# Kernel optimization log

Measured on AMD Instinct MI355X. Metric: run time of the kernel, lower is better.

## Reference

```python
import jax, jax.numpy as jnp
import numpy as np

B, S, D, E, H, TOPK = 4, 1024, 512, 8, 1536, 2
NORM_EPS = 1e-5

def _ln(x, w, b, eps=1e-5):
    m = jnp.mean(x, -1, keepdims=True)
    v = jnp.var(x, -1, keepdims=True)  # biased var, as torch LayerNorm
    return (x - m) * jax.lax.rsqrt(v + eps) * w + b

def _modulate(x, shift, scale):
    return x * (1 + scale[:, None, :]) + shift[:, None, :]

def setup_inputs() -> dict:
    key = jax.random.key(0)
    ks = jax.random.split(key, 14)
    s = 0.02
    return dict(
        x=jax.random.normal(ks[0], (B, S, D), jnp.float32),
        c=jax.random.normal(ks[1], (B, D), jnp.float32),
        W_ada=jax.random.normal(ks[2], (D, 6 * D), jnp.float32) * s,
        b_ada=jax.random.normal(ks[3], (6 * D,), jnp.float32) * 0.1,
        Wq=jax.random.normal(ks[4], (D, D), jnp.float32) * s,
        Wk=jax.random.normal(ks[5], (D, D), jnp.float32) * s,
        Wv=jax.random.normal(ks[6], (D, D), jnp.float32) * s,
        Wo=jax.random.normal(ks[7], (D, D), jnp.float32) * s,
        qn_w=jnp.ones((D,), jnp.float32), qn_b=jnp.zeros((D,), jnp.float32),
        kn_w=jnp.ones((D,), jnp.float32), kn_b=jnp.zeros((D,), jnp.float32),
        an_w=jnp.ones((D,), jnp.float32), an_b=jnp.zeros((D,), jnp.float32),
        fn_w=jnp.ones((D,), jnp.float32), fn_b=jnp.zeros((D,), jnp.float32),
        Wr=jax.random.normal(ks[8], (D, E), jnp.float32) * s,
        br=jnp.zeros((E,), jnp.float32),
        W1=jax.random.normal(ks[9], (E, D, H), jnp.float32) * s,
        W2=jax.random.normal(ks[10], (E, H, D), jnp.float32) * s,
        W3=jax.random.normal(ks[11], (E, D, H), jnp.float32) * s,
    )

def reference(x, c, W_ada, b_ada, Wq, Wk, Wv, Wo, qn_w, qn_b, kn_w, kn_b,
              an_w, an_b, fn_w, fn_b, Wr, br, W1, W2, W3):
    # adaLN conditioning: SiLU -> Linear -> 6 chunks
    mods = jax.nn.silu(c) @ W_ada + b_ada          # (B, 6D)
    sh_msa, sc_msa, g_msa, sh_mlp, sc_mlp, g_mlp = jnp.split(mods, 6, axis=1)

    # Attention (source attends over the FEATURE dim: scores are (B, D, D))
    h = _modulate(_ln(x, an_w, an_b, NORM_EPS), sh_msa, sc_msa)
    q = _ln(h @ Wq, qn_w, qn_b)
    k = _ln(h @ Wk, kn_w, kn_b)
    v = h @ Wv
    scores = jnp.einsum('bsd,bse->bde', q, k)      # (B, D, D), no 1/sqrt scale (as source)
    A = jax.nn.softmax(scores, axis=-1)
    attn = jnp.einsum('bde,bse->bsd', A, v) @ Wo   # (B, S, D)
    x = x + g_msa[:, None, :] * attn

    # MoE feed-forward (top-2 routing; output REPLACES x, no residual/gate per source)
    xm = _modulate(_ln(x, fn_w, fn_b, NORM_EPS), sh_mlp, sc_mlp)
    logits = xm @ Wr + br                          # (B, S, E)
    # F.normalize default dim=1 -> L2 normalize over the SEQUENCE axis (faithful)
    nrm = jnp.sqrt(jnp.sum(logits * logits, axis=1, keepdims=True))
    logits = logits / jnp.maximum(nrm, 1e-12)
    probs = jax.nn.softmax(logits, axis=-1)        # (B, S, E)
    vals, idx = jax.lax.top_k(probs, TOPK)

    T = B * S
    xf = xm.reshape(T, D)
    # dense combine weights: zero for unselected experts (same math as gather/scatter-add)
    wden = jnp.zeros((T, E), xf.dtype).at[jnp.arange(T)[:, None], idx.reshape(T, TOPK)].set(vals.reshape(T, TOPK))
    h1 = jnp.einsum('td,edh->teh', xf, W1)
    h3 = jnp.einsum('td,edh->teh', xf, W3)
    y = jnp.einsum('teh,ehd->ted', jnp.sin(h1) * h3, W2)  # sin-gated FFN per expert
    moe = jnp.einsum('ted,te->td', y, wden).reshape(B, S, D)

    avg = probs.mean(axis=0)                       # mean over batch dim only (faithful): (S, E)
    aux = jnp.sum((1.0 / E - avg) ** 2)
    return moe, aux
```

## Files before the change

kernel.cpp:

```cpp
#include <hip/hip_runtime.h>
#include <math.h>

#define NB 4
#define NS 1024
#define ND 512
#define NE 8
#define NH 1536
#define NT 4096
#define D6 3072

typedef _Float16 half_t;
typedef _Float16 f16x8 __attribute__((ext_vector_type(8)));
typedef _Float16 f16x4 __attribute__((ext_vector_type(4)));
typedef float    f32x4 __attribute__((ext_vector_type(4)));

#define LDH 40
#define LDC 136
#define TM_MAX 71

__device__ __forceinline__ void gld16(const void* g, void* l) {
  __builtin_amdgcn_global_load_lds((const __attribute__((address_space(1))) char*)g,
                                   (__attribute__((address_space(3))) char*)l, 16, 0, 0);
}

__device__ __forceinline__ int resolve_tile(const int* __restrict__ offs, int t,
                                            int& e_out, int& m0_out) {
  int acc = 0, found = 0, ee = 0, mm = 0;
  #pragma unroll
  for (int q = 0; q < NE; ++q) {
    int ne_q = offs[q + 1] - offs[q];
    int te = (ne_q + 127) >> 7;
    if (!found && t < acc + te) { ee = q; mm = (t - acc) << 7; found = 1; }
    acc += te;
  }
  e_out = ee; m0_out = mm;
  return found;
}

__global__ __launch_bounds__(256) void k_ada(const float* __restrict__ c,
    const float* __restrict__ Wada, const float* __restrict__ bada,
    float* __restrict__ mods)
{
  __shared__ float sc[ND];
  __shared__ float part[256];
  int tid = threadIdx.x;
  int blk = blockIdx.x;
  int o0 = blk * 64;
  int b = o0 / D6;
  int j0 = o0 - b * D6;
  for (int d = tid; d < ND; d += 256) {
    float v = c[b * ND + d];
    sc[d] = v / (1.f + expf(-v));
  }
  __syncthreads();
  int j = j0 + (tid & 63);
  int kc = tid >> 6;
  float acc = 0.f;
  #pragma unroll 8
  for (int d = kc * 128; d < kc * 128 + 128; ++d)
    acc += sc[d] * Wada[(size_t)d * D6 + j];
  part[tid] = acc;
  __syncthreads();
  if (tid < 64) {
    float r = part[tid] + part[tid + 64] + part[tid + 128] + part[tid + 192]
            + bada[j0 + tid];
    mods[b * D6 + j0 + tid] = r;
  }
}

__global__ __launch_bounds__(256) void k_lnmod(const float* X, int xstride,
    float* Yf, half_t* Yh, half_t* Yl, int ystride,
    const float* __restrict__ w, const float* __restrict__ b,
    const float* __restrict__ mods, int sh_off, int sc_off,
    const float* __restrict__ Wr, const float* __restrict__ br,
    float* __restrict__ logits)
{
  __shared__ float red[16];
  __shared__ float red2[32];
  int tid = threadIdx.x;
  int row = blockIdx.x;
  int batch = row >> 10;
  const float* xr = X + (size_t)row * xstride;
  float x0 = xr[tid], x1 = xr[tid + 256];
  float s = x0 + x1, q = x0 * x0 + x1 * x1;
  #pragma unroll
  for (int off = 32; off > 0; off >>= 1) { s += __shfl_down(s, off, 64); q += __shfl_down(q, off, 64); }
  if ((tid & 63) == 0) { red[tid >> 6] = s; red[8 + (tid >> 6)] = q; }
  __syncthreads();
  if (tid == 0) {
    float S = red[0] + red[1] + red[2] + red[3];
    float Q = red[8] + red[9] + red[10] + red[11];
    float mean = S * (1.f / (float)ND);
    float var = Q * (1.f / (float)ND) - mean * mean;
    red[0] = mean; red[1] = rsqrtf(var + 1e-5f);
  }
  __syncthreads();
  float mean = red[0], rstd = red[1];
  int d0 = tid, d1 = tid + 256;
  float y0 = (x0 - mean) * rstd * w[d0] + b[d0];
  float y1 = (x1 - mean) * rstd * w[d1] + b[d1];
  if (mods) {
    const float* mb = mods + batch * D6;
    y0 = y0 * (1.f + mb[sc_off + d0]) + mb[sh_off + d0];
    y1 = y1 * (1.f + mb[sc_off + d1]) + mb[sh_off + d1];
  }
  size_t o0 = (size_t)row * ystride + d0, o1 = (size_t)row * ystride + d1;
  if (Yf) { Yf[o0] = y0; Yf[o1] = y1; }
  if (Yh) {
    half_t h0 = (half_t)y0, h1 = (half_t)y1;
    Yh[o0] = h0; Yh[o1] = h1;
    if (Yl) { Yl[o0] = (half_t)(y0 - (float)h0); Yl[o1] = (half_t)(y1 - (float)h1); }
  }
  if (Wr) {
    float p[8];
    float4 wa = *(const float4*)(Wr + d0 * 8);
    float4 wb = *(const float4*)(Wr + d0 * 8 + 4);
    float4 wc = *(const float4*)(Wr + d1 * 8);
    float4 wd = *(const float4*)(Wr + d1 * 8 + 4);
    p[0] = y0 * wa.x + y1 * wc.x; p[1] = y0 * wa.y + y1 * wc.y;
    p[2] = y0 * wa.z + y1 * wc.z; p[3] = y0 * wa.w + y1 * wc.w;
    p[4] = y0 * wb.x + y1 * wd.x; p[5] = y0 * wb.y + y1 * wd.y;
    p[6] = y0 * wb.z + y1 * wd.z; p[7] = y0 * wb.w + y1 * wd.w;
    #pragma unroll
    for (int off = 32; off > 0; off >>= 1)
      #pragma unroll
      for (int e = 0; e < 8; ++e) p[e] += __shfl_down(p[e], off, 64);
    if ((tid & 63) == 0) {
      #pragma unroll
      for (int e = 0; e < 8; ++e) red2[(tid >> 6) * 8 + e] = p[e];
    }
    __syncthreads();
    if (tid < 8)
      logits[(size_t)row * 8 + tid] = red2[tid] + red2[8 + tid] + red2[16 + tid]
                                    + red2[24 + tid] + br[tid];
  }
}

__global__ __launch_bounds__(256) void k_lnqk(float* QKV,
    const float* __restrict__ qw, const float* __restrict__ qb,
    const float* __restrict__ kw, const float* __restrict__ kb)
{
  __shared__ float red[16];
  int tid = threadIdx.x;
  int row = blockIdx.x >> 1;
  int h = blockIdx.x & 1;
  const float* w = h ? kw : qw;
  const float* b = h ? kb : qb;
  float* xr = QKV + (size_t)row * 1536 + h * 512;
  float x0 = xr[tid], x1 = xr[tid + 256];
  float s = x0 + x1, q = x0 * x0 + x1 * x1;
  #pragma unroll
  for (int off = 32; off > 0; off >>= 1) { s += __shfl_down(s, off, 64); q += __shfl_down(q, off, 64); }
  if ((tid & 63) == 0) { red[tid >> 6] = s; red[8 + (tid >> 6)] = q; }
  __syncthreads();
  if (tid == 0) {
    float S = red[0] + red[1] + red[2] + red[3];
    float Q = red[8] + red[9] + red[10] + red[11];
    float mean = S * (1.f / (float)ND);
    float var = Q * (1.f / (float)ND) - mean * mean;
    red[0] = mean; red[1] = rsqrtf(var + 1e-5f);
  }
  __syncthreads();
  float mean = red[0], rstd = red[1];
  xr[tid]       = (x0 - mean) * rstd * w[tid] + b[tid];
  xr[tid + 256] = (x1 - mean) * rstd * w[tid + 256] + b[tid + 256];
}

__global__ __launch_bounds__(256) void k_tsplit2(const float* __restrict__ QKV,
    half_t* __restrict__ H0, half_t* __restrict__ L0)
{
  __shared__ float tile[32][33];
  int z = blockIdx.z;
  half_t* outH = H0 + (size_t)z * 4194304;
  half_t* outL = L0 + (size_t)z * 4194304;
  int col0 = z * 512;
  int s0 = blockIdx.x * 32, c0 = blockIdx.y * 32;
  int tid = threadIdx.x;
  int r = tid >> 5, c = tid & 31;
  #pragma unroll
  for (int p = 0; p < 4; ++p)
    tile[r + p * 8][c] = QKV[(size_t)(s0 + r + p * 8) * 1536 + col0 + c0 + c];
  __syncthreads();
  #pragma unroll
  for (int p = 0; p < 4; ++p) {
    float v = tile[c][r + p * 8];
    half_t h = (half_t)v;
    size_t o = (size_t)(c0 + r + p * 8) * NT + s0 + c;
    outH[o] = h; outL[o] = (half_t)(v - (float)h);
  }
}

__global__ __launch_bounds__(256) void k_wsplit4(const float* __restrict__ Wq,
    const float* __restrict__ Wk, const float* __restrict__ Wv,
    const float* __restrict__ Wo, half_t* __restrict__ outH, half_t* __restrict__ outL)
{
  __shared__ float tile[32][33];
  int z = blockIdx.z;
  const float* W = (z == 0) ? Wq : (z == 1) ? Wk : (z == 2) ? Wv : Wo;
  int rowoff = z * 512;
  int k0 = blockIdx.x * 32, n0 = blockIdx.y * 32;
  int tid = threadIdx.x;
  int r = tid >> 5, c = tid & 31;
  #pragma unroll
  for (int p = 0; p < 4; ++p)
    tile[r + p * 8][c] = W[(size_t)(k0 + r + p * 8) * ND + n0 + c];
  __syncthreads();
  #pragma unroll
  for (int p = 0; p < 4; ++p) {
    float v = tile[c][r + p * 8];
    half_t h = (half_t)v;
    size_t o = (size_t)(rowoff + n0 + r + p * 8) * ND + k0 + c;
    outH[o] = h; outL[o] = (half_t)(v - (float)h);
  }
}

__global__ __launch_bounds__(256) void k_vsplit(const float* __restrict__ QKV,
    half_t* __restrict__ Vh, half_t* __restrict__ Vl)
{
  int i = blockIdx.x * 256 + threadIdx.x;
  int s = i >> 7, c = (i & 127) * 4;
  float4 v = *(const float4*)(QKV + (size_t)s * 1536 + 1024 + c);
  f16x4 h, l;
  h[0] = (half_t)v.x; l[0] = (half_t)(v.x - (float)h[0]);
  h[1] = (half_t)v.y; l[1] = (half_t)(v.y - (float)h[1]);
  h[2] = (half_t)v.z; l[2] = (half_t)(v.z - (float)h[2]);
  h[3] = (half_t)v.w; l[3] = (half_t)(v.w - (float)h[3]);
  *(f16x4*)(Vh + (size_t)s * ND + c) = h;
  *(f16x4*)(Vl + (size_t)s * ND + c) = l;
}

template<int MODE>
__global__ __launch_bounds__(256) void k_gemm_hl(
    const half_t* __restrict__ Ah, const half_t* __restrict__ Al, long long sAz,
    const half_t* __restrict__ Bh, const half_t* __restrict__ Bl, long long sBz,
    int lda, int ldb, int K,
    float* __restrict__ Cf, half_t* __restrict__ Ch, half_t* __restrict__ Cl,
    long long sCz, int ldc,
    const float* __restrict__ xres, const float* __restrict__ mods)
{
  int z = blockIdx.z;
  int m0 = blockIdx.x * 128, n0 = blockIdx.y * 128;
  __shared__ __align__(16) char smem[40960];
  half_t* Ash = (half_t*)smem;
  half_t* Asl = (half_t*)(smem + 10240);
  half_t* Bsh = (half_t*)(smem + 20480);
  half_t* Bsl = (half_t*)(smem + 30720);
  int tid = threadIdx.x;
  int lane = tid & 63, w = tid >> 6;
  int wm = (w >> 1) * 64, wn = (w & 1) * 64;
  int qd = lane >> 4, md = lane & 15;
  int rA0 = tid >> 2, sA0 = (tid & 3) * 8;
  int rA1 = rA0 + 64;

  const half_t* pAh0 = Ah + z * sAz + (size_t)(m0 + rA0) * lda + sA0;
  const half_t* pAh1 = Ah + z * sAz + (size_t)(m0 + rA1) * lda + sA0;
  const half_t* pAl0 = Al + z * sAz + (size_t)(m0 + rA0) * lda + sA0;
  const half_t* pAl1 = Al + z * sAz + (size_t)(m0 + rA1) * lda + sA0;
  const half_t* pBh0 = Bh + z * sBz + (size_t)(n0 + rA0) * ldb + sA0;
  const half_t* pBh1 = Bh + z * sBz + (size_t)(n0 + rA1) * ldb + sA0;
  const half_t* pBl0 = Bl + z * sBz + (size_t)(n0 + rA0) * ldb + sA0;
  const half_t* pBl1 = Bl + z * sBz + (size_t)(n0 + rA1) * ldb + sA0;

  f32x4 acc[4][4];
  #pragma unroll
  for (int i = 0; i < 4; ++i)
    #pragma unroll
    for (int j = 0; j < 4; ++j)
      #pragma unroll
      for (int p = 0; p < 4; ++p) acc[i][j][p] = 0.f;

  f16x8 rah0 = *(const f16x8*)pAh0, rah1 = *(const f16x8*)pAh1;
  f16x8 ral0 = *(const f16x8*)pAl0, ral1 = *(const f16x8*)pAl1;
  f16x8 rbh0 = *(const f16x8*)pBh0, rbh1 = *(const f16x8*)pBh1;
  f16x8 rbl0 = *(const f16x8*)pBl0, rbl1 = *(const f16x8*)pBl1;

  int iters = K >> 5;
  #pragma unroll 1
  for (int it = 0; it < iters; ++it) {
    __syncthreads();
    *(f16x8*)(Ash + rA0 * LDH + sA0) = rah0;
    *(f16x8*)(Ash + rA1 * LDH + sA0) = rah1;
    *(f16x8*)(Asl + rA0 * LDH + sA0) = ral0;
    *(f16x8*)(Asl + rA1 * LDH + sA0) = ral1;
    *(f16x8*)(Bsh + rA0 * LDH + sA0) = rbh0;
    *(f16x8*)(Bsh + rA1 * LDH + sA0) = rbh1;
    *(f16x8*)(Bsl + rA0 * LDH + sA0) = rbl0;
    *(f16x8*)(Bsl + rA1 * LDH + sA0) = rbl1;
    __syncthreads();
    if (it < iters - 1) {
      int k1 = (it + 1) * 32;
      rah0 = *(const f16x8*)(pAh0 + k1); rah1 = *(const f16x8*)(pAh1 + k1);
      ral0 = *(const f16x8*)(pAl0 + k1); ral1 = *(const f16x8*)(pAl1 + k1);
      rbh0 = *(const f16x8*)(pBh0 + k1); rbh1 = *(const f16x8*)(pBh1 + k1);
      rbl0 = *(const f16x8*)(pBl0 + k1); rbl1 = *(const f16x8*)(pBl1 + k1);
    }
    f16x8 ah[4], al[4], bh[4], bl[4];
    #pragma unroll
    for (int i = 0; i < 4; ++i) {
      ah[i] = *(const f16x8*)(Ash + (wm + 16 * i + md) * LDH + qd * 8);
      al[i] = *(const f16x8*)(Asl + (wm + 16 * i + md) * LDH + qd * 8);
    }
    #pragma unroll
    for (int j = 0; j < 4; ++j) {
      bh[j] = *(const f16x8*)(Bsh + (wn + 16 * j + md) * LDH + qd * 8);
      bl[j] = *(const f16x8*)(Bsl + (wn + 16 * j + md) * LDH + qd * 8);
    }
    #pragma unroll
    for (int i = 0; i < 4; ++i)
      #pragma unroll
      for (int j = 0; j < 4; ++j) {
        acc[i][j] = __builtin_amdgcn_mfma_f32_16x16x32_f16(ah[i], bh[j], acc[i][j], 0, 0, 0);
        acc[i][j] = __builtin_amdgcn_mfma_f32_16x16x32_f16(ah[i], bl[j], acc[i][j], 0, 0, 0);
        acc[i][j] = __builtin_amdgcn_mfma_f32_16x16x32_f16(al[i], bh[j], acc[i][j], 0, 0, 0);
      }
  }

  if (MODE == 1) {
    half_t* Cs = (half_t*)smem;
    __syncthreads();
    #pragma unroll
    for (int i = 0; i < 4; ++i)
      #pragma unroll
      for (int j = 0; j < 4; ++j)
        #pragma unroll
        for (int p = 0; p < 4; ++p)
          Cs[(wm + 16 * i + qd * 4 + p) * LDC + wn + 16 * j + md] = (half_t)acc[i][j][p];
    __syncthreads();
    #pragma unroll
    for (int it2 = 0; it2 < 8; ++it2) {
      int chunk = it2 * 256 + tid;
      int r = chunk >> 4, c8 = (chunk & 15) * 8;
      *(f16x8*)(Ch + z * sCz + (size_t)(m0 + r) * ldc + n0 + c8) = *(const f16x8*)(Cs + r * LDC + c8);
    }
    __syncthreads();
    #pragma unroll
    for (int i = 0; i < 4; ++i)
      #pragma unroll
      for (int j = 0; j < 4; ++j)
        #pragma unroll
        for (int p = 0; p < 4; ++p) {
          float v = acc[i][j][p];
          half_t h = (half_t)v;
          Cs[(wm + 16 * i + qd * 4 + p) * LDC + wn + 16 * j + md] = (half_t)(v - (float)h);
        }
    __syncthreads();
    #pragma unroll
    for (int it2 = 0; it2 < 8; ++it2) {
      int chunk = it2 * 256 + tid;
      int r = chunk >> 4, c8 = (chunk & 15) * 8;
      *(f16x8*)(Cl + z * sCz + (size_t)(m0 + r) * ldc + n0 + c8) = *(const f16x8*)(Cs + r * LDC + c8);
    }
  } else {
    #pragma unroll
    for (int i = 0; i < 4; ++i)
      #pragma unroll
      for (int p = 0; p < 4; ++p) {
        int r = m0 + wm + 16 * i + qd * 4 + p;
        float* cp = Cf + z * sCz + (size_t)r * ldc + n0 + wn + md;
        if (MODE == 2) {
          int batch = r >> 10;
          const float* mb = mods + batch * D6 + 2 * ND;
          const float* xp = xres + (size_t)r * ldc + n0 + wn + md;
          #pragma unroll
          for (int j = 0; j < 4; ++j) {
            int col = wn + md + 16 * j;
            cp[16 * j] = xp[16 * j] + mb[n0 + col] * acc[i][j][p];
          }
        } else {
          #pragma unroll
          for (int j = 0; j < 4; ++j) cp[16 * j] = acc[i][j][p];
        }
      }
  }
}

__global__ __launch_bounds__(256) void k_softmax512_sum4(const float* __restrict__ SC4,
    half_t* __restrict__ Ph, half_t* __restrict__ Pl)
{
  __shared__ float red[16];
  int tid = threadIdx.x;
  int row = blockIdx.x;
  int b = row >> 9, d = row & 511;
  const float* r0 = SC4 + ((size_t)(b * 4 + 0) << 18) + (size_t)d * ND;
  const float* r1 = SC4 + ((size_t)(b * 4 + 1) << 18) + (size_t)d * ND;
  const float* r2 = SC4 + ((size_t)(b * 4 + 2) << 18) + (size_t)d * ND;
  const float* r3 = SC4 + ((size_t)(b * 4 + 3) << 18) + (size_t)d * ND;
  float x0 = r0[tid] + r1[tid] + r2[tid] + r3[tid];
  float x1 = r0[tid + 256] + r1[tid + 256] + r2[tid + 256] + r3[tid + 256];
  float m = fmaxf(x0, x1);
  #pragma unroll
  for (int off = 32; off > 0; off >>= 1) m = fmaxf(m, __shfl_down(m, off, 64));
  if ((tid & 63) == 0) red[tid >> 6] = m;
  __syncthreads();
  if (tid == 0) red[0] = fmaxf(fmaxf(red[0], red[1]), fmaxf(red[2], red[3]));
  __syncthreads();
  m = red[0];
  float e0 = expf(x0 - m), e1 = expf(x1 - m);
  float s = e0 + e1;
  #pragma unroll
  for (int off = 32; off > 0; off >>= 1) s += __shfl_down(s, off, 64);
  if ((tid & 63) == 0) red[8 + (tid >> 6)] = s;
  __syncthreads();
  if (tid == 0) red[8] = red[8] + red[9] + red[10] + red[11];
  __syncthreads();
  float inv = 1.f / red[8];
  float p0 = e0 * inv, p1 = e1 * inv;
  size_t base = (size_t)row * ND;
  half_t h0 = (half_t)p0, h1 = (half_t)p1;
  Ph[base + tid] = h0;       Pl[base + tid] = (half_t)(p0 - (float)h0);
  Ph[base + tid + 256] = h1; Pl[base + tid + 256] = (half_t)(p1 - (float)h1);
}

__global__ __launch_bounds__(256) void k_colnorm(const float* __restrict__ logits,
    float* __restrict__ nrm, int* __restrict__ cnt)
{
  __shared__ float red[8];
  int tid = threadIdx.x;
  if (blockIdx.x == 0 && tid < 16) cnt[tid] = 0;
  int b = blockIdx.x >> 3, e = blockIdx.x & 7;
  float acc = 0.f;
  for (int s = tid; s < NS; s += 256) {
    float l = logits[((size_t)(b << 10) + s) * NE + e];
    acc += l * l;
  }
  #pragma unroll
  for (int off = 32; off > 0; off >>= 1) acc += __shfl_down(acc, off, 64);
  if ((tid & 63) == 0) red[tid >> 6] = acc;
  __syncthreads();
  if (tid == 0) nrm[b * NE + e] = sqrtf(red[0] + red[1] + red[2] + red[3]);
}

__global__ __launch_bounds__(256) void k_top2(const float* __restrict__ logits,
    const float* __restrict__ nrm, float* __restrict__ probs,
    float* __restrict__ wsel, int* __restrict__ isel, int* __restrict__ cnt)
{
  int t = blockIdx.x * 256 + threadIdx.x;
  int b = t >> 10;
  float p[NE];
  float mx = -1e30f;
  #pragma unroll
  for (int e = 0; e < NE; ++e) {
    float l = logits[t * NE + e] / fmaxf(nrm[b * NE + e], 1e-12f);
    p[e] = l;
    mx = fmaxf(mx, l);
  }
  float s = 0.f;
  #pragma unroll
  for (int e = 0; e < NE; ++e) { p[e] = expf(p[e] - mx); s += p[e]; }
  float inv = 1.f / s;
  #pragma unroll
  for (int e = 0; e < NE; ++e) { p[e] *= inv; probs[t * NE + e] = p[e]; }
  int i1 = 0;
  #pragma unroll
  for (int e = 1; e < NE; ++e) if (p[e] > p[i1]) i1 = e;
  int i2 = (i1 == 0) ? 1 : 0;
  #pragma unroll
  for (int e = 0; e < NE; ++e) if (e != i1 && p[e] > p[i2]) i2 = e;
  wsel[t * 2] = p[i1]; wsel[t * 2 + 1] = p[i2];
  isel[t * 2] = i1;    isel[t * 2 + 1] = i2;
  atomicAdd(&cnt[i1], 1); atomicAdd(&cnt[i2], 1);
}

__global__ void k_scan(const int* __restrict__ cnt, int* __restrict__ offs)
{
  if (threadIdx.x == 0) {
    int a = 0;
    for (int e = 0; e < NE; ++e) { offs[e] = a; a += cnt[e]; }
    offs[NE] = a;
  }
}

__global__ __launch_bounds__(256) void k_fill(const int* __restrict__ isel,
    const int* __restrict__ offs, int* __restrict__ cnt2,
    int* __restrict__ list, int* __restrict__ inv)
{
  int idx = blockIdx.x * 256 + threadIdx.x;
  int e = isel[idx];
  int pos = atomicAdd(&cnt2[e], 1);
  int slot = offs[e] + pos;
  list[slot] = idx >> 1;
  inv[idx] = slot;
}

__global__ __launch_bounds__(256) void k_aux(const float* __restrict__ probs,
    float* __restrict__ outAux)
{
  __shared__ float red[8];
  int tid = threadIdx.x;
  float acc = 0.f;
  for (int s = tid; s < NS; s += 256) {
    #pragma unroll
    for (int e = 0; e < NE; ++e) {
      float a = probs[(size_t)s * NE + e] + probs[(size_t)(NS + s) * NE + e]
              + probs[(size_t)(2 * NS + s) * NE + e] + probs[(size_t)(3 * NS + s) * NE + e];
      float d = 0.125f - a * 0.25f;
      acc += d * d;
    }
  }
  #pragma unroll
  for (int off = 32; off > 0; off >>= 1) acc += __shfl_down(acc, off, 64);
  if ((tid & 63) == 0) red[tid >> 6] = acc;
  __syncthreads();
  if (tid == 0) *outAux = red[0] + red[1] + red[2] + red[3];
}

__global__ __launch_bounds__(256) void k_tcast13(const float* __restrict__ W1,
    const float* __restrict__ W3, half_t* __restrict__ W1t, half_t* __restrict__ W3t)
{
  __shared__ float tile[32][33];
  int z = blockIdx.z;
  int sel = z >> 3, e = z & 7;
  const float* We = (sel ? W3 : W1) + (size_t)e * ND * NH;
  half_t* Wte = (sel ? W3t : W1t) + (size_t)e * ND * NH;
  int k0 = blockIdx.x * 32, n0 = blockIdx.y * 32;
  int tid = threadIdx.x;
  int r = tid >> 5, c = tid & 31;
  #pragma unroll
  for (int p = 0; p < 4; ++p)
    tile[r + p * 8][c] = We[(size_t)(k0 + r + p * 8) * NH + n0 + c];
  __syncthreads();
  #pragma unroll
  for (int p = 0; p < 4; ++p)
    Wte[(size_t)(n0 + r + p * 8) * ND + k0 + c] = (half_t)tile[c][r + p * 8];
}

__global__ __launch_bounds__(256) void k_tcastW2(const float* __restrict__ W,
    half_t* __restrict__ Wt)
{
  __shared__ float tile[32][33];
  const float* We = W + (size_t)blockIdx.z * NH * ND;
  half_t* Wte = Wt + (size_t)blockIdx.z * NH * ND;
  int k0 = blockIdx.x * 32, n0 = blockIdx.y * 32;
  int tid = threadIdx.x;
  int r = tid >> 5, c = tid & 31;
  #pragma unroll
  for (int p = 0; p < 4; ++p)
    tile[r + p * 8][c] = We[(size_t)(k0 + r + p * 8) * ND + n0 + c];
  __syncthreads();
  #pragma unroll
  for (int p = 0; p < 4; ++p)
    Wte[(size_t)(n0 + r + p * 8) * NH + k0 + c] = (half_t)tile[c][r + p * 8];
}

__global__ __launch_bounds__(256, 3) void k_ffn_fused(const half_t* __restrict__ xmh,
    const half_t* __restrict__ W1t, const half_t* __restrict__ W3t,
    const int* __restrict__ list, const int* __restrict__ offs,
    half_t* __restrict__ gate)
{
  int bx = blockIdx.x;
  int n0 = (bx % 12) * 128;
  int t  = bx / 12;
  int e, m0;
  if (!resolve_tile(offs, t, e, m0)) return;
  int base = offs[e], ne = offs[e + 1] - base;

  __shared__ __align__(16) char smem[49664];
  half_t* Sh = (half_t*)smem;
  int* rowt = (int*)(smem + 49152);
  int tid = threadIdx.x;
  if (tid < 128) {
    int rr = m0 + tid;
    rowt[tid] = (rr < ne) ? list[base + rr] : 0;
  }
  __syncthreads();

  int lane = tid & 63, w = tid >> 6;
  int wm = (w >> 1) * 64, wn = (w & 1) * 64;
  int qd = lane >> 4, md = lane & 15;
  int rA0 = tid >> 2;
  int sw = (((tid & 3) ^ ((tid >> 3) & 3)) << 3);
  int tok0 = rowt[rA0], tok1 = rowt[rA0 + 64];

  const half_t* gA0  = xmh + (size_t)tok0 * ND + sw;
  const half_t* gA1  = xmh + (size_t)tok1 * ND + sw;
  const half_t* gB10 = W1t + ((size_t)e * NH + n0 + rA0) * ND + sw;
  const half_t* gB11 = gB10 + (size_t)64 * ND;
  const half_t* gB30 = W3t + ((size_t)e * NH + n0 + rA0) * ND + sw;
  const half_t* gB31 = gB30 + (size_t)64 * ND;

  char* dA  = smem + w * 1024;
  char* dB1 = smem + 16384 + w * 1024;
  char* dB3 = smem + 32768 + w * 1024;

  f32x4 acc1[4][4], acc3[4][4];
  #pragma unroll
  for (int i = 0; i < 4; ++i)
    #pragma unroll
    for (int j = 0; j < 4; ++j)
      #pragma unroll
      for (int p = 0; p < 4; ++p) { acc1[i][j][p] = 0.f; acc3[i][j][p] = 0.f; }

  int swq  = ((qd ^ ((md >> 1) & 3)) << 3);
  int aoff = (wm + md) * 32 + swq;
  int boff = (wn + md) * 32 + swq;

#define FFN_STAGE(p, kk) do { int kb_ = (kk); int pb_ = (p) * 8192;          \
    gld16(gA0  + kb_, dA  + pb_); gld16(gA1  + kb_, dA  + pb_ + 4096);       \
    gld16(gB10 + kb_, dB1 + pb_); gld16(gB11 + kb_, dB1 + pb_ + 4096);       \
    gld16(gB30 + kb_, dB3 + pb_); gld16(gB31 + kb_, dB3 + pb_ + 4096); } while (0)

  FFN_STAGE(0, 0);
  asm volatile("s_waitcnt vmcnt(0)\ns_barrier" ::: "memory");
  int cur = 0;
  #pragma unroll 1
  for (int it = 0; it < 16; ++it) {
    if (it + 1 < 16) FFN_STAGE(cur ^ 1, (it + 1) * 32);
    const half_t* As  = Sh + cur * 4096;
    const half_t* B1s = Sh + 8192  + cur * 4096;
    const half_t* B3s = Sh + 16384 + cur * 4096;
    f16x8 a[4];
    #pragma unroll
    for (int i = 0; i < 4; ++i) a[i] = *(const f16x8*)(As + aoff + i * 512);
    #pragma unroll
    for (int j = 0; j < 4; ++j) {
      f16x8 b1 = *(const f16x8*)(B1s + boff + j * 512);
      f16x8 b3 = *(const f16x8*)(B3s + boff + j * 512);
      #pragma unroll
      for (int i = 0; i < 4; ++i) {
        acc1[i][j] = __builtin_amdgcn_mfma_f32_16x16x32_f16(a[i], b1, acc1[i][j], 0, 0, 0);
        acc3[i][j] = __builtin_amdgcn_mfma_f32_16x16x32_f16(a[i], b3, acc3[i][j], 0, 0, 0);
      }
    }
    asm volatile("s_waitcnt vmcnt(0)\ns_barrier" ::: "memory");
    cur ^= 1;
  }
#undef FFN_STAGE

  half_t* Cs = (half_t*)smem;
  #pragma unroll
  for (int i = 0; i < 4; ++i)
    #pragma unroll
    for (int j = 0; j < 4; ++j)
      #pragma unroll
      for (int p = 0; p < 4; ++p) {
        int rr = wm + 16 * i + qd * 4 + p;
        int cc = wn + 16 * j + md;
        Cs[rr * LDC + cc] = (half_t)(__sinf(acc1[i][j][p]) * acc3[i][j][p]);
      }
  __syncthreads();
  #pragma unroll
  for (int it = 0; it < 8; ++it) {
    int chunk = it * 256 + tid;
    int rr = chunk >> 4, c8 = (chunk & 15) * 8;
    if (m0 + rr < ne) {
      *(f16x8*)(gate + (size_t)(base + m0 + rr) * NH + n0 + c8) = *(const f16x8*)(Cs + rr * LDC + c8);
    }
  }
}

__global__ __launch_bounds__(256, 4) void k_moe2_mfma(const half_t* __restrict__ gate,
    const half_t* __restrict__ W2t, const int* __restrict__ offs,
    float* __restrict__ P)
{
  int bx = blockIdx.x;
  int n0 = (bx & 3) * 128;
  int t = bx >> 2;
  int e, m0;
  if (!resolve_tile(offs, t, e, m0)) return;
  int base = offs[e], ne = offs[e + 1] - base;

  __shared__ __align__(16) char smem[32768];
  half_t* Sh = (half_t*)smem;
  int tid = threadIdx.x;
  int lane = tid & 63, w = tid >> 6;
  int wm = (w >> 1) * 64, wn = (w & 1) * 64;
  int qd = lane >> 4, md = lane & 15;
  int rA0 = tid >> 2;
  int sw = (((tid & 3) ^ ((tid >> 3) & 3)) << 3);

  int ar0 = m0 + rA0;      if (ar0 >= ne) ar0 = ne - 1;
  int ar1 = m0 + rA0 + 64; if (ar1 >= ne) ar1 = ne - 1;
  const half_t* gA0 = gate + (size_t)(base + ar0) * NH + sw;
  const half_t* gA1 = gate + (size_t)(base + ar1) * NH + sw;
  const half_t* gB0 = W2t + ((size_t)e * ND + n0 + rA0) * NH + sw;
  const half_t* gB1 = gB0 + (size_t)64 * NH;

  char* dA = smem + w * 1024;
  char* dB = smem + 16384 + w * 1024;

  f32x4 acc[4][4];
  #pragma unroll
  for (int i = 0; i < 4; ++i)
    #pragma unroll
    for (int j = 0; j < 4; ++j)
      #pragma unroll
      for (int p = 0; p < 4; ++p) acc[i][j][p] = 0.f;

  int swq  = ((qd ^ ((md >> 1) & 3)) << 3);
  int aoff = (wm + md) * 32 + swq;
  int boff = (wn + md) * 32 + swq;

#define MOE2_STAGE(p, kk) do { int kb_ = (kk); int pb_ = (p) * 8192;         \
    gld16(gA0 + kb_, dA + pb_); gld16(gA1 + kb_, dA + pb_ + 4096);           \
    gld16(gB0 + kb_, dB + pb_); gld16(gB1 + kb_, dB + pb_ + 4096); } while (0)

  MOE2_STAGE(0, 0);
  asm volatile("s_waitcnt vmcnt(0)\ns_barrier" ::: "memory");
  int cur = 0;
  #pragma unroll 1
  for (int it = 0; it < 48; ++it) {
    if (it + 1 < 48) MOE2_STAGE(cur ^ 1, (it + 1) * 32);
    const half_t* As = Sh + cur * 4096;
    const half_t* Bs = Sh + 8192 + cur * 4096;
    f16x8 a[4];
    #pragma unroll
    for (int i = 0; i < 4; ++i) a[i] = *(const f16x8*)(As + aoff + i * 512);
    #pragma unroll
    for (int j = 0; j < 4; ++j) {
      f16x8 b = *(const f16x8*)(Bs + boff + j * 512);
      #pragma unroll
      for (int i = 0; i < 4; ++i)
        acc[i][j] = __builtin_amdgcn_mfma_f32_16x16x32_f16(a[i], b, acc[i][j], 0, 0, 0);
    }
    asm volatile("s_waitcnt vmcnt(0)\ns_barrier" ::: "memory");
    cur ^= 1;
  }
#undef MOE2_STAGE

  #pragma unroll
  for (int i = 0; i < 4; ++i)
    #pragma unroll
    for (int p = 0; p < 4; ++p) {
      int gr = m0 + wm + 16 * i + qd * 4 + p;
      if (gr < ne) {
        float* pp = P + (size_t)(base + gr) * ND + n0 + wn + md;
        #pragma unroll
        for (int j = 0; j < 4; ++j)
          pp[16 * j] = acc[i][j][p];
      }
    }
}

__global__ __launch_bounds__(256) void k_moe_reduce(const float* __restrict__ P,
    const int* __restrict__ inv, const float* __restrict__ wsel,
    float* __restrict__ out)
{
  int i = blockIdx.x * 256 + threadIdx.x;
  int t = i >> 7, d4 = i & 127;
  int s1 = inv[t * 2], s2 = inv[t * 2 + 1];
  float w1 = wsel[t * 2], w2 = wsel[t * 2 + 1];
  const float4* P4 = (const float4*)P;
  float4 a = P4[(size_t)s1 * 128 + d4];
  float4 b = P4[(size_t)s2 * 128 + d4];
  float4 o;
  o.x = w1 * a.x + w2 * b.x;
  o.y = w1 * a.y + w2 * b.y;
  o.z = w1 * a.z + w2 * b.z;
  o.w = w1 * a.w + w2 * b.w;
  ((float4*)out)[i] = o;
}

static const size_t BO_MODS  = 0;
static const size_t BO_HH    = 65536;
static const size_t BO_HL2   = 4259840;
static const size_t BO_PH    = 4259840;
static const size_t BO_PL    = 6357056;
static const size_t BO_WALLH = 8454144;
static const size_t BO_WALLL = 10551296;
static const size_t BO_QKV   = 12648448;
static const size_t BO_A0H   = 12648448;
static const size_t BO_A0L   = 16842752;
static const size_t BO_SC4   = 21037056;
static const size_t BO_X2    = 21037056;
static const size_t BO_XM    = 29425664;
static const size_t BO_QTH   = 37814272;
static const size_t BO_QTL   = 42008576;
static const size_t BO_KTH   = 46202880;
static const size_t BO_KTL   = 50397184;
static const size_t BO_VH    = 54591488;
static const size_t BO_VL    = 58785792;
static const size_t BO_W1T   = 37814272;
static const size_t BO_XMH   = 50397184;
static const size_t BO_W3T   = 65536;
static const size_t BO_GATE  = 12648448;
static const size_t BO_W2T   = 65536;
static const size_t BO_P     = 37814272;
static const size_t BO_LOGI  = 62980096;
static const size_t BO_NRM   = 63111168;
static const size_t BO_PROB  = 63111296;
static const size_t BO_WSEL  = 63242368;
static const size_t BO_INTS  = 63307904;

extern "C" void kernel_launch(void* const* d_in, const int* in_sizes, int n_in,
                              void* d_out, int out_size, void* d_ws, size_t ws_size,
                              hipStream_t stream)
{
  const float* x    = (const float*)d_in[0];
  const float* c    = (const float*)d_in[1];
  const float* Wada = (const float*)d_in[2];
  const float* bada = (const float*)d_in[3];
  const float* Wq   = (const float*)d_in[4];
  const float* Wk   = (const float*)d_in[5];
  const float* Wv   = (const float*)d_in[6];
  const float* Wo   = (const float*)d_in[7];
  const float* qn_w = (const float*)d_in[8];
  const float* qn_b = (const float*)d_in[9];
  const float* kn_w = (const float*)d_in[10];
  const float* kn_b = (const float*)d_in[11];
  const float* an_w = (const float*)d_in[12];
  const float* an_b = (const float*)d_in[13];
  const float* fn_w = (const float*)d_in[14];
  const float* fn_b = (const float*)d_in[15];
  const float* Wr   = (const float*)d_in[16];
  const float* br   = (const float*)d_in[17];
  const float* W1   = (const float*)d_in[18];
  const float* W2   = (const float*)d_in[19];
  const float* W3   = (const float*)d_in[20];
  float* out = (float*)d_out;
  char*  ws8 = (char*)d_ws;
  float* MODS = (float*)(ws8 + BO_MODS);
  half_t* Hh = (half_t*)(ws8 + BO_HH),   *Hl = (half_t*)(ws8 + BO_HL2);
  half_t* Ph = (half_t*)(ws8 + BO_PH),   *Pl = (half_t*)(ws8 + BO_PL);
  half_t* WALLH = (half_t*)(ws8 + BO_WALLH), *WALLL = (half_t*)(ws8 + BO_WALLL);
  half_t* WoTh = WALLH + (size_t)1536 * ND,  *WoTl = WALLL + (size_t)1536 * ND;
  float* QKV = (float*)(ws8 + BO_QKV);
  half_t* A0h = (half_t*)(ws8 + BO_A0H), *A0l = (half_t*)(ws8 + BO_A0L);
  float* SC4 = (float*)(ws8 + BO_SC4);
  float* X2  = (float*)(ws8 + BO_X2);
  float* XM  = (float*)(ws8 + BO_XM);
  half_t* qTh = (half_t*)(ws8 + BO_QTH), *qTl = (half_t*)(ws8 + BO_QTL);
  half_t* kTh = (half_t*)(ws8 + BO_KTH), *kTl = (half_t*)(ws8 + BO_KTL);
  half_t* Vh  = (half_t*)(ws8 + BO_VH),  *Vl  = (half_t*)(ws8 + BO_VL);
  half_t* W1T = (half_t*)(ws8 + BO_W1T);
  half_t* W3T = (half_t*)(ws8 + BO_W3T);
  half_t* W2T = (half_t*)(ws8 + BO_W2T);
  half_t* XMH = (half_t*)(ws8 + BO_XMH);
  half_t* GATEH = (half_t*)(ws8 + BO_GATE);
  float* PBUF = (float*)(ws8 + BO_P);
  float* LOGI = (float*)(ws8 + BO_LOGI);
  float* NRM  = (float*)(ws8 + BO_NRM);
  float* PROB = (float*)(ws8 + BO_PROB);
  float* WSEL = (float*)(ws8 + BO_WSEL);
  int* ib   = (int*)(ws8 + BO_INTS);
  int* isel = ib;
  int* cnt  = ib + 8192;
  int* cnt2 = ib + 8200;
  int* offs = ib + 8208;
  int* list = ib + 8224;
  int* inv  = ib + 16416;

  k_ada<<<192, 256, 0, stream>>>(c, Wada, bada, MODS);
  k_wsplit4<<<dim3(16, 16, 4), 256, 0, stream>>>(Wq, Wk, Wv, Wo, WALLH, WALLL);
  k_lnmod<<<NT, 256, 0, stream>>>(x, ND, nullptr, Hh, Hl, ND, an_w, an_b, MODS, 0, 512,
                                  nullptr, nullptr, nullptr);
  k_gemm_hl<0><<<dim3(32, 12, 1), 256, 0, stream>>>(Hh, Hl, 0, WALLH, WALLL, 0,
      ND, ND, ND, QKV, nullptr, nullptr, 0, 1536, nullptr, nullptr);
  k_lnqk<<<2 * NT, 256, 0, stream>>>(QKV, qn_w, qn_b, kn_w, kn_b);
  k_tsplit2<<<dim3(128, 16, 2), 256, 0, stream>>>(QKV, qTh, qTl);
  k_vsplit<<<2048, 256, 0, stream>>>(QKV, Vh, Vl);
  k_gemm_hl<0><<<dim3(4, 4, 16), 256, 0, stream>>>(qTh, qTl, 256, kTh, kTl, 256,
      NT, NT, 256, SC4, nullptr, nullptr, 262144, ND, nullptr, nullptr);
  k_softmax512_sum4<<<2048, 256, 0, stream>>>(SC4, Ph, Pl);
  k_gemm_hl<1><<<dim3(8, 4, 4), 256, 0, stream>>>(Vh, Vl, 524288, Ph, Pl, 262144,
      ND, ND, ND, nullptr, A0h, A0l, 524288, ND, nullptr, nullptr);
  k_gemm_hl<2><<<dim3(32, 4, 1), 256, 0, stream>>>(A0h, A0l, 0, WoTh, WoTl, 0,
      ND, ND, ND, X2, nullptr, nullptr, 0, ND, x, MODS);
  k_lnmod<<<NT, 256, 0, stream>>>(X2, ND, XM, XMH, nullptr, ND, fn_w, fn_b, MODS, 1536, 2048,
                                  Wr, br, LOGI);
  k_colnorm<<<32, 256, 0, stream>>>(LOGI, NRM, cnt);
  k_top2<<<16, 256, 0, stream>>>(LOGI, NRM, PROB, WSEL, isel, cnt);
  k_scan<<<1, 64, 0, stream>>>(cnt, offs);
  k_fill<<<32, 256, 0, stream>>>(isel, offs, cnt2, list, inv);
  k_aux<<<1, 256, 0, stream>>>(PROB, out + (size_t)NT * ND);
  k_tcast13<<<dim3(16, 48, 16), 256, 0, stream>>>(W1, W3, W1T, W3T);
  k_ffn_fused<<<TM_MAX * 12, 256, 0, stream>>>(XMH, W1T, W3T, list, offs, GATEH);
  k_tcastW2<<<dim3(48, 16, 8), 256, 0, stream>>>(W2, W2T);
  k_moe2_mfma<<<TM_MAX * 4, 256, 0, stream>>>(GATEH, W2T, offs, PBUF);
  k_moe_reduce<<<2048, 256, 0, stream>>>(PBUF, inv, WSEL, out);
}
```

Measured before the change: 473.2 us.

## Double-buffer split-fp16 GEMM via direct global-to-LDS loads with XOR swizzle

The k_gemm_hl main loop now loads tiles straight into LDS with global_load_lds instead of staging them through registers, double-buffers the shared tiles, and uses an XOR-swizzled unpadded layout in place of the padded LDH stride. This aims to overlap the next K-slice's loads with the current MFMAs, cut register pressure, and avoid LDS bank conflicts. It also adds a launch-bounds occupancy hint of 2 and grows shared memory to 64KB, which may limit how many blocks fit per CU.

Result: faster. 457.6 us (-3.3%).

```diff
diff --git a/kernel.cpp b/kernel.cpp
--- a/kernel.cpp
+++ b/kernel.cpp
@@ -14,7 +14,6 @@
 typedef _Float16 f16x4 __attribute__((ext_vector_type(4)));
 typedef float    f32x4 __attribute__((ext_vector_type(4)));
 
-#define LDH 40
 #define LDC 136
 #define TM_MAX 71
 
@@ -230,7 +229,7 @@
 }
 
 template<int MODE>
-__global__ __launch_bounds__(256) void k_gemm_hl(
+__global__ __launch_bounds__(256, 2) void k_gemm_hl(
     const half_t* __restrict__ Ah, const half_t* __restrict__ Al, long long sAz,
     const half_t* __restrict__ Bh, const half_t* __restrict__ Bl, long long sBz,
     int lda, int ldb, int K,
@@ -240,26 +239,28 @@
 {
   int z = blockIdx.z;
   int m0 = blockIdx.x * 128, n0 = blockIdx.y * 128;
-  __shared__ __align__(16) char smem[40960];
-  half_t* Ash = (half_t*)smem;
-  half_t* Asl = (half_t*)(smem + 10240);
-  half_t* Bsh = (half_t*)(smem + 20480);
-  half_t* Bsl = (half_t*)(smem + 30720);
+  __shared__ __align__(16) char smem[65536];
+  half_t* Sh = (half_t*)smem;
   int tid = threadIdx.x;
   int lane = tid & 63, w = tid >> 6;
   int wm = (w >> 1) * 64, wn = (w & 1) * 64;
   int qd = lane >> 4, md = lane & 15;
-  int rA0 = tid >> 2, sA0 = (tid & 3) * 8;
-  int rA1 = rA0 + 64;
-
-  const half_t* pAh0 = Ah + z * sAz + (size_t)(m0 + rA0) * lda + sA0;
-  const half_t* pAh1 = Ah + z * sAz + (size_t)(m0 + rA1) * lda + sA0;
-  const half_t* pAl0 = Al + z * sAz + (size_t)(m0 + rA0) * lda + sA0;
-  const half_t* pAl1 = Al + z * sAz + (size_t)(m0 + rA1) * lda + sA0;
-  const half_t* pBh0 = Bh + z * sBz + (size_t)(n0 + rA0) * ldb + sA0;
-  const half_t* pBh1 = Bh + z * sBz + (size_t)(n0 + rA1) * ldb + sA0;
-  const half_t* pBl0 = Bl + z * sBz + (size_t)(n0 + rA0) * ldb + sA0;
-  const half_t* pBl1 = Bl + z * sBz + (size_t)(n0 + rA1) * ldb + sA0;
+  int rA0 = tid >> 2;
+  int sw = (((tid & 3) ^ ((tid >> 3) & 3)) << 3);
+
+  const half_t* pAh0 = Ah + z * sAz + (size_t)(m0 + rA0) * lda + sw;
+  const half_t* pAh1 = pAh0 + (size_t)64 * lda;
+  const half_t* pAl0 = Al + z * sAz + (size_t)(m0 + rA0) * lda + sw;
+  const half_t* pAl1 = pAl0 + (size_t)64 * lda;
+  const half_t* pBh0 = Bh + z * sBz + (size_t)(n0 + rA0) * ldb + sw;
+  const half_t* pBh1 = pBh0 + (size_t)64 * ldb;
+  const half_t* pBl0 = Bl + z * sBz + (size_t)(n0 + rA0) * ldb + sw;
+  const half_t* pBl1 = pBl0 + (size_t)64 * ldb;
+
+  char* dAh = smem + w * 1024;
+  char* dAl = smem + 16384 + w * 1024;
+  char* dBh = smem + 32768 + w * 1024;
+  char* dBl = smem + 49152 + w * 1024;
 
   f32x4 acc[4][4];
   #pragma unroll
@@ -269,41 +270,37 @@
       #pragma unroll
       for (int p = 0; p < 4; ++p) acc[i][j][p] = 0.f;
 
-  f16x8 rah0 = *(const f16x8*)pAh0, rah1 = *(const f16x8*)pAh1;
-  f16x8 ral0 = *(const f16x8*)pAl0, ral1 = *(const f16x8*)pAl1;
-  f16x8 rbh0 = *(const f16x8*)pBh0, rbh1 = *(const f16x8*)pBh1;
-  f16x8 rbl0 = *(const f16x8*)pBl0, rbl1 = *(const f16x8*)pBl1;
+  int swq  = ((qd ^ ((md >> 1) & 3)) << 3);
+  int aoff = (wm + md) * 32 + swq;
+  int boff = (wn + md) * 32 + swq;
+
+#define GEMM_STAGE(p, kk) do { int kb_ = (kk); int pb_ = (p) * 8192;         \
+    gld16(pAh0 + kb_, dAh + pb_); gld16(pAh1 + kb_, dAh + pb_ + 4096);       \
+    gld16(pAl0 + kb_, dAl + pb_); gld16(pAl1 + kb_, dAl + pb_ + 4096);       \
+    gld16(pBh0 + kb_, dBh + pb_); gld16(pBh1 + kb_, dBh + pb_ + 4096);       \
+    gld16(pBl0 + kb_, dBl + pb_); gld16(pBl1 + kb_, dBl + pb_ + 4096); } while (0)
 
   int iters = K >> 5;
+  GEMM_STAGE(0, 0);
+  asm volatile("s_waitcnt vmcnt(0)\ns_barrier" ::: "memory");
+  int cur = 0;
   #pragma unroll 1
   for (int it = 0; it < iters; ++it) {
-    __syncthreads();
-    *(f16x8*)(Ash + rA0 * LDH + sA0) = rah0;
-    *(f16x8*)(Ash + rA1 * LDH + sA0) = rah1;
-    *(f16x8*)(Asl + rA0 * LDH + sA0) = ral0;
-    *(f16x8*)(Asl + rA1 * LDH + sA0) = ral1;
-    *(f16x8*)(Bsh + rA0 * LDH + sA0) = rbh0;
-    *(f16x8*)(Bsh + rA1 * LDH + sA0) = rbh1;
-    *(f16x8*)(Bsl + rA0 * LDH + sA0) = rbl0;
-    *(f16x8*)(Bsl + rA1 * LDH + sA0) = rbl1;
-    __syncthreads();
-    if (it < iters - 1) {
-      int k1 = (it + 1) * 32;
-      rah0 = *(const f16x8*)(pAh0 + k1); rah1 = *(const f16x8*)(pAh1 + k1);
-      ral0 = *(const f16x8*)(pAl0 + k1); ral1 = *(const f16x8*)(pAl1 + k1);
-      rbh0 = *(const f16x8*)(pBh0 + k1); rbh1 = *(const f16x8*)(pBh1 + k1);
-      rbl0 = *(const f16x8*)(pBl0 + k1); rbl1 = *(const f16x8*)(pBl1 + k1);
-    }
+    if (it + 1 < iters) GEMM_STAGE(cur ^ 1, (it + 1) * 32);
+    const half_t* Ash = Sh + cur * 4096;
+    const half_t* Asl = Sh + 8192  + cur * 4096;
+    const half_t* Bsh = Sh + 16384 + cur * 4096;
+    const half_t* Bsl = Sh + 24576 + cur * 4096;
     f16x8 ah[4], al[4], bh[4], bl[4];
     #pragma unroll
     for (int i = 0; i < 4; ++i) {
-      ah[i] = *(const f16x8*)(Ash + (wm + 16 * i + md) * LDH + qd * 8);
-      al[i] = *(const f16x8*)(Asl + (wm + 16 * i + md) * LDH + qd * 8);
+      ah[i] = *(const f16x8*)(Ash + aoff + i * 512);
+      al[i] = *(const f16x8*)(Asl + aoff + i * 512);
     }
     #pragma unroll
     for (int j = 0; j < 4; ++j) {
-      bh[j] = *(const f16x8*)(Bsh + (wn + 16 * j + md) * LDH + qd * 8);
-      bl[j] = *(const f16x8*)(Bsl + (wn + 16 * j + md) * LDH + qd * 8);
+      bh[j] = *(const f16x8*)(Bsh + boff + j * 512);
+      bl[j] = *(const f16x8*)(Bsl + boff + j * 512);
     }
     #pragma unroll
     for (int i = 0; i < 4; ++i)
@@ -313,7 +310,10 @@
         acc[i][j] = __builtin_amdgcn_mfma_f32_16x16x32_f16(ah[i], bl[j], acc[i][j], 0, 0, 0);
         acc[i][j] = __builtin_amdgcn_mfma_f32_16x16x32_f16(al[i], bh[j], acc[i][j], 0, 0, 0);
       }
-  }
+    asm volatile("s_waitcnt vmcnt(0)\ns_barrier" ::: "memory");
+    cur ^= 1;
+  }
+#undef GEMM_STAGE
 
   if (MODE == 1) {
     half_t* Cs = (half_t*)smem;
```
